# Optimization experiments

Measured on AMD Instinct MI355X. Metric: run time of the kernel, lower is better.

Reference implementation:

```python
import jax, jax.numpy as jnp
import numpy as np

B, N, D, S, H, ITERS = 128, 4096, 64, 7, 128, 3
EPS = 1e-8
LN_EPS = 1e-5


def _ln(x, g, b):
    mu = jnp.mean(x, axis=-1, keepdims=True)
    var = jnp.mean(jnp.square(x - mu), axis=-1, keepdims=True)
    return (x - mu) * jax.lax.rsqrt(var + LN_EPS) * g + b


def setup_inputs() -> dict:
    key = jax.random.key(0)
    ks = jax.random.split(key, 20)
    xav = lambda k, shp: jax.random.normal(k, shp, jnp.float32) * (2.0 / sum(shp[-2:])) ** 0.5
    inp = {
        "inputs": jax.random.normal(ks[0], (B, N, D), jnp.float32),
        "noise_bg": jax.random.normal(ks[1], (B, 1, D), jnp.float32),
        "noise_fg": jax.random.normal(ks[2], (B, S - 1, D), jnp.float32),
        "ln_in_g": jnp.ones((D,), jnp.float32), "ln_in_b": jnp.zeros((D,), jnp.float32),
        "ln_slot_g": jnp.ones((D,), jnp.float32), "ln_slot_b": jnp.zeros((D,), jnp.float32),
        "ln_mlp_g": jnp.ones((D,), jnp.float32), "ln_mlp_b": jnp.zeros((D,), jnp.float32),
        "Wq": xav(ks[3], (D, D)), "Wk": xav(ks[4], (D, D)), "Wv": xav(ks[5], (D, D)),
        "W_ih": xav(ks[6], (3 * D, D)), "W_hh": xav(ks[7], (3 * D, D)),
        "b_ih": jnp.zeros((3 * D,), jnp.float32), "b_hh": jnp.zeros((3 * D,), jnp.float32),
        "mlp_w1": xav(ks[8], (H, D)), "mlp_b1": jnp.zeros((H,), jnp.float32),
        "mlp_w2": xav(ks[9], (D, H)), "mlp_b2": jnp.zeros((D,), jnp.float32),
        "slots_bg_mu": xav(ks[10], (1, 1, D)),
        "slots_bg_log_sigma": xav(ks[11], (1, 1, D)),
        "slots_mu": xav(ks[12], (1, 1, D)),
        "slots_log_sigma": xav(ks[13], (1, 1, D)),
    }
    return inp


def _gru(x, h, W_ih, W_hh, b_ih, b_hh):
    # x, h: [M, D]; PyTorch GRUCell math, gate order r, z, n
    gi = x @ W_ih.T + b_ih
    gh = h @ W_hh.T + b_hh
    i_r, i_z, i_n = jnp.split(gi, 3, axis=-1)
    h_r, h_z, h_n = jnp.split(gh, 3, axis=-1)
    r = jax.nn.sigmoid(i_r + h_r)
    z = jax.nn.sigmoid(i_z + h_z)
    n = jnp.tanh(i_n + r * h_n)
    return (1.0 - z) * n + z * h


def reference(inputs, noise_bg, noise_fg, ln_in_g, ln_in_b, ln_slot_g, ln_slot_b,
              ln_mlp_g, ln_mlp_b, Wq, Wk, Wv, W_ih, W_hh, b_ih, b_hh,
              mlp_w1, mlp_b1, mlp_w2, mlp_b2,
              slots_bg_mu, slots_bg_log_sigma, slots_mu, slots_log_sigma):
    x = _ln(inputs, ln_in_g, ln_in_b)          # [B, N, D]
    k = jnp.einsum('bnd,ed->bne', x, Wk)       # [B, N, D]
    v = jnp.einsum('bnd,ed->bne', x, Wv)

    bg = slots_bg_mu + jnp.exp(slots_bg_log_sigma) * noise_bg   # [B, 1, D]
    fg = slots_mu + jnp.exp(slots_log_sigma) * noise_fg          # [B, S-1, D]
    slots = jnp.concatenate([bg, fg], axis=1)                    # [B, S, D]

    scale = D ** (-0.5)
    for _ in range(ITERS):
        slots_prev = slots
        s = _ln(slots, ln_slot_g, ln_slot_b)
        q = jnp.einsum('bsd,ed->bse', s, Wq)                     # [B, S, D]
        logits = scale * jnp.einsum('bnd,bsd->bns', k, q)        # [B, N, S]
        attn = jax.nn.softmax(logits, axis=-1) + EPS             # softmax over slots
        attn = attn / jnp.sum(attn, axis=1, keepdims=True)       # renorm over inputs
        updates = jnp.einsum('bns,bnd->bsd', attn, v)            # [B, S, D]
        h = _gru(updates.reshape(B * S, D), slots_prev.reshape(B * S, D),
                 W_ih, W_hh, b_ih, b_hh).reshape(B, S, D)
        m = _ln(h, ln_mlp_g, ln_mlp_b)
        m = jax.nn.relu(m @ mlp_w1.T + mlp_b1) @ mlp_w2.T + mlp_b2
        slots = h + m
    return slots
```

## Files before the change

kernel.cpp:

```cpp
#include <hip/hip_runtime.h>

#define BB 128
#define NN 4096
#define DD 64
#define SS 7
#define HH 128
#define N_ITERS 3
#define EPS_ATTN 1e-8f
#define LN_EPS 1e-5f

typedef unsigned short ushortT;
using short8  = __attribute__((ext_vector_type(8))) short;
using floatx4 = __attribute__((ext_vector_type(4))) float;

__device__ __forceinline__ float bf2f(unsigned u) {
    return __builtin_bit_cast(float, (u & 0xffffu) << 16);
}
__device__ __forceinline__ ushortT f2bf(float f) {
    unsigned x = __builtin_bit_cast(unsigned, f);
    x = x + 0x7fff + ((x >> 16) & 1);
    return (ushortT)(x >> 16);
}
__device__ __forceinline__ void wave_stats64(float x, float& mu, float& var) {
    float s1 = x, s2 = x * x;
#pragma unroll
    for (int off = 32; off > 0; off >>= 1) {
        s1 += __shfl_xor(s1, off);
        s2 += __shfl_xor(s2, off);
    }
    mu  = s1 * (1.f / 64.f);
    var = s2 * (1.f / 64.f) - mu * mu;
}

__global__ void prep_w(const float* __restrict__ Wih, const float* __restrict__ Whh,
                       const float* __restrict__ w1, const float* __restrict__ w2,
                       const float* __restrict__ Wv,
                       float* __restrict__ WihT, float* __restrict__ WhhT,
                       float* __restrict__ w1T, float* __restrict__ w2T,
                       float* __restrict__ WvT) {
    int i = blockIdx.x * 256 + threadIdx.x;
    if (i < 12288) {
        int e = i >> 6, d = i & 63;
        WihT[d * 192 + e] = Wih[i];
    } else if (i < 24576) {
        int j = i - 12288; int e = j >> 6, d = j & 63;
        WhhT[d * 192 + e] = Whh[j];
    } else if (i < 32768) {
        int j = i - 24576; int e = j >> 6, d = j & 63;
        w1T[d * 128 + e] = w1[j];
    } else if (i < 40960) {
        int j = i - 32768; int e = j >> 7, h = j & 127;
        w2T[h * 64 + e] = w2[j];
    } else if (i < 45056) {
        int j = i - 40960; int d = j >> 6, e = j & 63;
        WvT[e * 64 + d] = Wv[j];
    }
}

__global__ __launch_bounds__(256) void attn_kernel(
    int first,
    const float* __restrict__ x,
    const float* __restrict__ lng, const float* __restrict__ lnb,
    ushortT* __restrict__ xnf,
    const float* __restrict__ qkbuf,
    float* __restrict__ pxn_p, float* __restrict__ den_p) {
    int t = threadIdx.x;
    int ck = blockIdx.x, b = ck >> 5;
    int w = t >> 6, lane = t & 63, m = lane & 15, qd = lane >> 4;
    int sub = t & 3, rr = t >> 2;
    __shared__ float   qk_lds[7][68];
    __shared__ ushortT xnT[64][136];
    __shared__ ushortT p_lds[16][136];
    __shared__ float   den_w[4][8];

    unsigned xw[2][8];
    if (first) {
        float4 g4[4], b4[4];
#pragma unroll
        for (int c = 0; c < 4; ++c) {
            g4[c] = *reinterpret_cast<const float4*>(lng + sub * 16 + c * 4);
            b4[c] = *reinterpret_cast<const float4*>(lnb + sub * 16 + c * 4);
        }
#pragma unroll
        for (int pass = 0; pass < 2; ++pass) {
            const float* xr = x + ((long)ck * 128 + pass * 64 + rr) * 64 + sub * 16;
            float4 xa[4];
#pragma unroll
            for (int c = 0; c < 4; ++c)
                xa[c] = *reinterpret_cast<const float4*>(xr + c * 4);
            float s1 = 0.f, s2 = 0.f;
#pragma unroll
            for (int c = 0; c < 4; ++c) {
                s1 += xa[c].x + xa[c].y + xa[c].z + xa[c].w;
                s2 += xa[c].x * xa[c].x + xa[c].y * xa[c].y +
                      xa[c].z * xa[c].z + xa[c].w * xa[c].w;
            }
            s1 += __shfl_xor(s1, 1); s2 += __shfl_xor(s2, 1);
            s1 += __shfl_xor(s1, 2); s2 += __shfl_xor(s2, 2);
            float mu = s1 * (1.f / 64.f);
            float var = s2 * (1.f / 64.f) - mu * mu;
            float rs = rsqrtf(var + LN_EPS);
#pragma unroll
            for (int c = 0; c < 4; ++c) {
                float n0 = (xa[c].x - mu) * rs * g4[c].x + b4[c].x;
                float n1 = (xa[c].y - mu) * rs * g4[c].y + b4[c].y;
                float n2 = (xa[c].z - mu) * rs * g4[c].z + b4[c].z;
                float n3 = (xa[c].w - mu) * rs * g4[c].w + b4[c].w;
                xw[pass][c * 2]     = (unsigned)f2bf(n0) | ((unsigned)f2bf(n1) << 16);
                xw[pass][c * 2 + 1] = (unsigned)f2bf(n2) | ((unsigned)f2bf(n3) << 16);
            }
            ushortT* xp = xnf + (long)ck * 8192 + pass * 4096 + t * 16;
            *reinterpret_cast<uint4*>(xp) =
                make_uint4(xw[pass][0], xw[pass][1], xw[pass][2], xw[pass][3]);
            *reinterpret_cast<uint4*>(xp + 8) =
                make_uint4(xw[pass][4], xw[pass][5], xw[pass][6], xw[pass][7]);
        }
    } else {
#pragma unroll
        for (int pass = 0; pass < 2; ++pass) {
            const ushortT* xp = xnf + (long)ck * 8192 + pass * 4096 + t * 16;
            uint4 u0 = *reinterpret_cast<const uint4*>(xp);
            uint4 u1 = *reinterpret_cast<const uint4*>(xp + 8);
            xw[pass][0] = u0.x; xw[pass][1] = u0.y;
            xw[pass][2] = u0.z; xw[pass][3] = u0.w;
            xw[pass][4] = u1.x; xw[pass][5] = u1.y;
            xw[pass][6] = u1.z; xw[pass][7] = u1.w;
        }
    }
    for (int i = t; i < 448; i += 256) qk_lds[i >> 6][i & 63] = qkbuf[b * 448 + i];
    __syncthreads();

    float dreg0 = 0.f, dreg1 = 0.f;
    int s0 = sub * 2;
#pragma unroll
    for (int pass = 0; pass < 2; ++pass) {
        int row = pass * 64 + rr;
#pragma unroll
        for (int j = 0; j < 16; ++j)
            xnT[sub * 16 + j][row] =
                (ushortT)(xw[pass][j >> 1] >> ((j & 1) * 16));
        float kx[16];
#pragma unroll
        for (int j = 0; j < 8; ++j) {
            kx[2 * j]     = bf2f(xw[pass][j]);
            kx[2 * j + 1] = bf2f(xw[pass][j] >> 16);
        }
        float lg[7];
#pragma unroll
        for (int s = 0; s < 7; ++s) {
            const float4* qp = reinterpret_cast<const float4*>(&qk_lds[s][sub << 4]);
            float acc = 0.f;
#pragma unroll
            for (int c = 0; c < 4; ++c) {
                float4 qv = qp[c];
                acc += kx[c * 4 + 0] * qv.x + kx[c * 4 + 1] * qv.y +
                       kx[c * 4 + 2] * qv.z + kx[c * 4 + 3] * qv.w;
            }
            lg[s] = acc;
        }
#pragma unroll
        for (int s = 0; s < 7; ++s) {
            lg[s] += __shfl_xor(lg[s], 1);
            lg[s] += __shfl_xor(lg[s], 2);
        }
        float mx = lg[0];
#pragma unroll
        for (int s = 1; s < 7; ++s) mx = fmaxf(mx, lg[s]);
        float sum = 0.f, ps[7];
#pragma unroll
        for (int s = 0; s < 7; ++s) { ps[s] = __expf(lg[s] - mx); sum += ps[s]; }
        float inv = 1.f / sum;
        float p0 = 0.f, p1 = 0.f;
#pragma unroll
        for (int s = 0; s < 7; ++s) {
            float pv = ps[s] * inv + EPS_ATTN;
            if (s == s0)     p0 = pv;
            if (s == s0 + 1) p1 = pv;
        }
        ushortT pb0 = f2bf(p0);
        p_lds[s0][row] = pb0;
        dreg0 += bf2f(pb0);
        if (sub < 3) {
            ushortT pb1 = f2bf(p1);
            p_lds[s0 + 1][row] = pb1;
            dreg1 += bf2f(pb1);
        }
    }
#pragma unroll
    for (int off = 4; off < 64; off <<= 1) {
        dreg0 += __shfl_xor(dreg0, off);
        dreg1 += __shfl_xor(dreg1, off);
    }
    if (lane < 4) {
        den_w[w][2 * lane] = dreg0;
        if (lane < 3) den_w[w][2 * lane + 1] = dreg1;
    }
    __syncthreads();

    floatx4 acc = (floatx4){0.f, 0.f, 0.f, 0.f};
#pragma unroll
    for (int ks = 0; ks < 4; ++ks) {
        short8 af = *reinterpret_cast<const short8*>(&p_lds[m][ks * 32 + qd * 8]);
        short8 bf = *reinterpret_cast<const short8*>(&xnT[w * 16 + m][ks * 32 + qd * 8]);
        acc = __builtin_amdgcn_mfma_f32_16x16x32_bf16(af, bf, acc, 0, 0, 0);
    }
#pragma unroll
    for (int r = 0; r < 4; ++r) {
        int s = qd * 4 + r;
        if (s < 7) pxn_p[((long)ck * 7 + s) * 64 + w * 16 + m] = acc[r];
    }
    if (t < 7) den_p[ck * 8 + t] = den_w[0][t] + den_w[1][t] + den_w[2][t] + den_w[3][t];
}

__global__ __launch_bounds__(448) void slot_update_q(
    int mode,
    const float* __restrict__ pxn_p, const float* __restrict__ den_p,
    float* __restrict__ slots,
    const float* __restrict__ nbg, const float* __restrict__ nfg,
    const float* __restrict__ bgmu, const float* __restrict__ bgls,
    const float* __restrict__ fmu, const float* __restrict__ fls,
    const float* __restrict__ WihT, const float* __restrict__ WhhT,
    const float* __restrict__ bih, const float* __restrict__ bhh,
    const float* __restrict__ lng, const float* __restrict__ lnb,
    const float* __restrict__ w1T, const float* __restrict__ b1,
    const float* __restrict__ w2T, const float* __restrict__ b2,
    const float* __restrict__ WvT, const float* __restrict__ Wk,
    const float* __restrict__ Wq,
    const float* __restrict__ sg, const float* __restrict__ sb,
    float* __restrict__ qkbuf, float* __restrict__ outp) {
    int b = blockIdx.x, t = threadIdx.x, s = t >> 6, l = t & 63;
    __shared__ float WqT[64 * 65];
    __shared__ float pxnL[7][64], updL[7][64], hprevL[7][64], mnL[7][64],
                     xnL[7][64], qL[7][64], m1L[7][128];
    if (mode != 2)
        for (int i = t; i < 4096; i += 448)
            WqT[(i & 63) * 65 + (i >> 6)] = Wq[i];
    float res;
    if (mode == 0) {
        float v;
        if (s == 0) v = bgmu[l] + __expf(bgls[l]) * nbg[b * 64 + l];
        else        v = fmu[l]  + __expf(fls[l])  * nfg[(b * 6 + s - 1) * 64 + l];
        res = v;
        __syncthreads();
    } else {
        float psum = 0.f, dsum = 0.f;
#pragma unroll 4
        for (int c = 0; c < 32; ++c) {
            psum += pxn_p[((long)(b * 32 + c) * 7 + s) * 64 + l];
            dsum += den_p[(b * 32 + c) * 8 + s];
        }
        pxnL[s][l] = psum;
        float hp = slots[(b * 7 + s) * 64 + l];
        hprevL[s][l] = hp;
        float nm = 0.f;
#pragma unroll 8
        for (int e = 0; e < 64; ++e) nm += pxnL[s][e] * WvT[e * 64 + l];
        updL[s][l] = nm / dsum;
        __syncthreads();
        float gi0 = bih[l], gi1 = bih[64 + l], gi2 = bih[128 + l];
        float gh0 = bhh[l], gh1 = bhh[64 + l], gh2 = bhh[128 + l];
#pragma unroll 8
        for (int d = 0; d < 64; ++d) {
            float u = updL[s][d], hh = hprevL[s][d];
            gi0 += u * WihT[d * 192 + l];
            gi1 += u * WihT[d * 192 + 64 + l];
            gi2 += u * WihT[d * 192 + 128 + l];
            gh0 += hh * WhhT[d * 192 + l];
            gh1 += hh * WhhT[d * 192 + 64 + l];
            gh2 += hh * WhhT[d * 192 + 128 + l];
        }
        float r = 1.f / (1.f + __expf(-(gi0 + gh0)));
        float z = 1.f / (1.f + __expf(-(gi1 + gh1)));
        float n = tanhf(gi2 + r * gh2);
        float h = (1.f - z) * n + z * hp;
        float mu, var;
        wave_stats64(h, mu, var);
        mnL[s][l] = (h - mu) * rsqrtf(var + LN_EPS) * lng[l] + lnb[l];
        float a0 = b1[l], a1 = b1[64 + l];
#pragma unroll 8
        for (int d = 0; d < 64; ++d) {
            float mv = mnL[s][d];
            a0 += mv * w1T[d * 128 + l];
            a1 += mv * w1T[d * 128 + 64 + l];
        }
        m1L[s][l]      = fmaxf(a0, 0.f);
        m1L[s][64 + l] = fmaxf(a1, 0.f);
        float a2 = b2[l];
#pragma unroll 8
        for (int h2 = 0; h2 < 128; ++h2) a2 += m1L[s][h2] * w2T[h2 * 64 + l];
        res = h + a2;
    }
    slots[(b * 7 + s) * 64 + l] = res;
    if (mode == 2) {
        outp[(b * 7 + s) * 64 + l] = res;
        return;
    }
    float mu, var;
    wave_stats64(res, mu, var);
    xnL[s][l] = (res - mu) * rsqrtf(var + LN_EPS) * sg[l] + sb[l];
    float qv = 0.f;
#pragma unroll 8
    for (int d = 0; d < 64; ++d) qv += xnL[s][d] * WqT[d * 65 + l];
    qL[s][l] = qv * 0.125f;
    float qk = 0.f;
#pragma unroll 8
    for (int e = 0; e < 64; ++e) qk += qL[s][e] * Wk[e * 64 + l];
    qkbuf[(b * 7 + s) * 64 + l] = qk;
}

extern "C" void kernel_launch(void* const* d_in, const int* in_sizes, int n_in,
                              void* d_out, int out_size, void* d_ws, size_t ws_size,
                              hipStream_t stream) {
    const float* inputs    = (const float*)d_in[0];
    const float* noise_bg  = (const float*)d_in[1];
    const float* noise_fg  = (const float*)d_in[2];
    const float* ln_in_g   = (const float*)d_in[3];
    const float* ln_in_b   = (const float*)d_in[4];
    const float* ln_slot_g = (const float*)d_in[5];
    const float* ln_slot_b = (const float*)d_in[6];
    const float* ln_mlp_g  = (const float*)d_in[7];
    const float* ln_mlp_b  = (const float*)d_in[8];
    const float* Wq        = (const float*)d_in[9];
    const float* Wk        = (const float*)d_in[10];
    const float* Wv        = (const float*)d_in[11];
    const float* W_ih      = (const float*)d_in[12];
    const float* W_hh      = (const float*)d_in[13];
    const float* b_ih      = (const float*)d_in[14];
    const float* b_hh      = (const float*)d_in[15];
    const float* mlp_w1    = (const float*)d_in[16];
    const float* mlp_b1    = (const float*)d_in[17];
    const float* mlp_w2    = (const float*)d_in[18];
    const float* mlp_b2    = (const float*)d_in[19];
    const float* sbg_mu    = (const float*)d_in[20];
    const float* sbg_ls    = (const float*)d_in[21];
    const float* s_mu      = (const float*)d_in[22];
    const float* s_ls      = (const float*)d_in[23];

    char* ws = (char*)d_ws;
    size_t off = 0;
    auto alloc = [&](size_t bytes) {
        void* p = ws + off;
        off += (bytes + 255) & ~(size_t)255;
        return p;
    };
    ushortT* xnf   = (ushortT*)alloc((size_t)BB * NN * 64 * 2);
    float* slots   = (float*)alloc(57344 * 4);
    float* qkbuf   = (float*)alloc(57344 * 4);
    float* pxn_p   = (float*)alloc((size_t)4096 * 7 * 64 * 4);
    float* den_p   = (float*)alloc(4096 * 8 * 4);
    float* WihT    = (float*)alloc(12288 * 4);
    float* WhhT    = (float*)alloc(12288 * 4);
    float* w1T     = (float*)alloc(8192 * 4);
    float* w2T     = (float*)alloc(8192 * 4);
    float* WvT     = (float*)alloc(4096 * 4);
    if (off > ws_size) return;

    prep_w<<<176, 256, 0, stream>>>(W_ih, W_hh, mlp_w1, mlp_w2, Wv,
                                    WihT, WhhT, w1T, w2T, WvT);
    slot_update_q<<<128, 448, 0, stream>>>(0, pxn_p, den_p, slots,
                                           noise_bg, noise_fg, sbg_mu, sbg_ls,
                                           s_mu, s_ls, WihT, WhhT, b_ih, b_hh,
                                           ln_mlp_g, ln_mlp_b, w1T, mlp_b1,
                                           w2T, mlp_b2, WvT, Wk, Wq,
                                           ln_slot_g, ln_slot_b,
                                           qkbuf, (float*)d_out);
    for (int it = 0; it < N_ITERS; ++it) {
        attn_kernel<<<4096, 256, 0, stream>>>((it == 0) ? 1 : 0,
                                              inputs, ln_in_g, ln_in_b,
                                              xnf, qkbuf, pxn_p, den_p);
        slot_update_q<<<128, 448, 0, stream>>>((it == N_ITERS - 1) ? 2 : 1,
                                               pxn_p, den_p, slots,
                                               noise_bg, noise_fg, sbg_mu, sbg_ls,
                                               s_mu, s_ls, WihT, WhhT, b_ih, b_hh,
                                               ln_mlp_g, ln_mlp_b, w1T, mlp_b1,
                                               w2T, mlp_b2, WvT, Wk, Wq,
                                               ln_slot_g, ln_slot_b,
                                               qkbuf, (float*)d_out);
    }
}
```

Before: 382.6 us.

## Compute attention logits with MFMA and split slot update into per-slot blocks

The attention kernel now computes key-query logits with bf16 MFMA instructions in place of scalar dot products plus shuffles. To support this, the row-to-lane layout is changed to an MFMA-friendly tile layout, and the transposed LDS buffer gets a 140 stride. The slot update kernel moves from 128 blocks of 448 threads to 896 blocks of 192 threads, one per slot, with WqT precomputed in prep_w. The qk buffer is stored transposed and padded to 8 slots. The logits now use a bf16-rounded query, which can shift precision slightly.

```diff
diff --git a/kernel.cpp b/kernel.cpp
--- a/kernel.cpp
+++ b/kernel.cpp
@@ -12,6 +12,7 @@
 typedef unsigned short ushortT;
 using short8  = __attribute__((ext_vector_type(8))) short;
 using floatx4 = __attribute__((ext_vector_type(4))) float;
+using uint4v  = __attribute__((ext_vector_type(4))) unsigned;
 
 __device__ __forceinline__ float bf2f(unsigned u) {
     return __builtin_bit_cast(float, (u & 0xffffu) << 16);
@@ -34,10 +35,10 @@
 
 __global__ void prep_w(const float* __restrict__ Wih, const float* __restrict__ Whh,
                        const float* __restrict__ w1, const float* __restrict__ w2,
-                       const float* __restrict__ Wv,
+                       const float* __restrict__ Wv, const float* __restrict__ Wq,
                        float* __restrict__ WihT, float* __restrict__ WhhT,
                        float* __restrict__ w1T, float* __restrict__ w2T,
-                       float* __restrict__ WvT) {
+                       float* __restrict__ WvT, float* __restrict__ WqT) {
     int i = blockIdx.x * 256 + threadIdx.x;
     if (i < 12288) {
         int e = i >> 6, d = i & 63;
@@ -54,6 +55,9 @@
     } else if (i < 45056) {
         int j = i - 40960; int d = j >> 6, e = j & 63;
         WvT[e * 64 + d] = Wv[j];
+    } else if (i < 49152) {
+        int j = i - 45056; int d = j >> 6, e = j & 63;
+        WqT[j] = Wq[e * 64 + d];
     }
 }
 
@@ -62,157 +66,181 @@
     const float* __restrict__ x,
     const float* __restrict__ lng, const float* __restrict__ lnb,
     ushortT* __restrict__ xnf,
-    const float* __restrict__ qkbuf,
+    const float* __restrict__ qkT,
     float* __restrict__ pxn_p, float* __restrict__ den_p) {
     int t = threadIdx.x;
     int ck = blockIdx.x, b = ck >> 5;
     int w = t >> 6, lane = t & 63, m = lane & 15, qd = lane >> 4;
-    int sub = t & 3, rr = t >> 2;
-    __shared__ float   qk_lds[7][68];
-    __shared__ ushortT xnT[64][136];
+    __shared__ float   qk_lds[512];
+    __shared__ ushortT xnT[64 * 140];
     __shared__ ushortT p_lds[16][136];
     __shared__ float   den_w[4][8];
 
+    for (int i = t; i < 512; i += 256) qk_lds[i] = qkT[b * 512 + i];
+
     unsigned xw[2][8];
     if (first) {
-        float4 g4[4], b4[4];
-#pragma unroll
-        for (int c = 0; c < 4; ++c) {
-            g4[c] = *reinterpret_cast<const float4*>(lng + sub * 16 + c * 4);
-            b4[c] = *reinterpret_cast<const float4*>(lnb + sub * 16 + c * 4);
-        }
-#pragma unroll
-        for (int pass = 0; pass < 2; ++pass) {
-            const float* xr = x + ((long)ck * 128 + pass * 64 + rr) * 64 + sub * 16;
-            float4 xa[4];
-#pragma unroll
-            for (int c = 0; c < 4; ++c)
-                xa[c] = *reinterpret_cast<const float4*>(xr + c * 4);
+        float4 g4[2][2], b4[2][2];
+#pragma unroll
+        for (int c = 0; c < 2; ++c) {
+            g4[c][0] = *reinterpret_cast<const float4*>(lng + c * 32 + qd * 8);
+            g4[c][1] = *reinterpret_cast<const float4*>(lng + c * 32 + qd * 8 + 4);
+            b4[c][0] = *reinterpret_cast<const float4*>(lnb + c * 32 + qd * 8);
+            b4[c][1] = *reinterpret_cast<const float4*>(lnb + c * 32 + qd * 8 + 4);
+        }
+#pragma unroll
+        for (int tile = 0; tile < 2; ++tile) {
+            long R = (long)ck * 128 + w * 32 + tile * 16 + m;
+            float4 xa[2][2];
+#pragma unroll
+            for (int c = 0; c < 2; ++c) {
+                xa[c][0] = *reinterpret_cast<const float4*>(x + R * 64 + c * 32 + qd * 8);
+                xa[c][1] = *reinterpret_cast<const float4*>(x + R * 64 + c * 32 + qd * 8 + 4);
+            }
             float s1 = 0.f, s2 = 0.f;
 #pragma unroll
-            for (int c = 0; c < 4; ++c) {
-                s1 += xa[c].x + xa[c].y + xa[c].z + xa[c].w;
-                s2 += xa[c].x * xa[c].x + xa[c].y * xa[c].y +
-                      xa[c].z * xa[c].z + xa[c].w * xa[c].w;
-            }
-            s1 += __shfl_xor(s1, 1); s2 += __shfl_xor(s2, 1);
-            s1 += __shfl_xor(s1, 2); s2 += __shfl_xor(s2, 2);
+            for (int c = 0; c < 2; ++c)
+#pragma unroll
+                for (int h = 0; h < 2; ++h) {
+                    float4 v = xa[c][h];
+                    s1 += v.x + v.y + v.z + v.w;
+                    s2 += v.x * v.x + v.y * v.y + v.z * v.z + v.w * v.w;
+                }
+            s1 += __shfl_xor(s1, 16); s2 += __shfl_xor(s2, 16);
+            s1 += __shfl_xor(s1, 32); s2 += __shfl_xor(s2, 32);
             float mu = s1 * (1.f / 64.f);
             float var = s2 * (1.f / 64.f) - mu * mu;
             float rs = rsqrtf(var + LN_EPS);
 #pragma unroll
-            for (int c = 0; c < 4; ++c) {
-                float n0 = (xa[c].x - mu) * rs * g4[c].x + b4[c].x;
-                float n1 = (xa[c].y - mu) * rs * g4[c].y + b4[c].y;
-                float n2 = (xa[c].z - mu) * rs * g4[c].z + b4[c].z;
-                float n3 = (xa[c].w - mu) * rs * g4[c].w + b4[c].w;
-                xw[pass][c * 2]     = (unsigned)f2bf(n0) | ((unsigned)f2bf(n1) << 16);
-                xw[pass][c * 2 + 1] = (unsigned)f2bf(n2) | ((unsigned)f2bf(n3) << 16);
-            }
-            ushortT* xp = xnf + (long)ck * 8192 + pass * 4096 + t * 16;
+            for (int c = 0; c < 2; ++c)
+#pragma unroll
+                for (int h = 0; h < 2; ++h) {
+                    float n0 = (xa[c][h].x - mu) * rs * g4[c][h].x + b4[c][h].x;
+                    float n1 = (xa[c][h].y - mu) * rs * g4[c][h].y + b4[c][h].y;
+                    float n2 = (xa[c][h].z - mu) * rs * g4[c][h].z + b4[c][h].z;
+                    float n3 = (xa[c][h].w - mu) * rs * g4[c][h].w + b4[c][h].w;
+                    xw[tile][c * 4 + h * 2]     = (unsigned)f2bf(n0) | ((unsigned)f2bf(n1) << 16);
+                    xw[tile][c * 4 + h * 2 + 1] = (unsigned)f2bf(n2) | ((unsigned)f2bf(n3) << 16);
+                }
+            ushortT* xp = xnf + (long)ck * 8192 + w * 2048 + tile * 1024 + lane * 16;
             *reinterpret_cast<uint4*>(xp) =
-                make_uint4(xw[pass][0], xw[pass][1], xw[pass][2], xw[pass][3]);
+                make_uint4(xw[tile][0], xw[tile][1], xw[tile][2], xw[tile][3]);
             *reinterpret_cast<uint4*>(xp + 8) =
-                make_uint4(xw[pass][4], xw[pass][5], xw[pass][6], xw[pass][7]);
+                make_uint4(xw[tile][4], xw[tile][5], xw[tile][6], xw[tile][7]);
         }
     } else {
 #pragma unroll
-        for (int pass = 0; pass < 2; ++pass) {
-            const ushortT* xp = xnf + (long)ck * 8192 + pass * 4096 + t * 16;
+        for (int tile = 0; tile < 2; ++tile) {
+            const ushortT* xp = xnf + (long)ck * 8192 + w * 2048 + tile * 1024 + lane * 16;
             uint4 u0 = *reinterpret_cast<const uint4*>(xp);
             uint4 u1 = *reinterpret_cast<const uint4*>(xp + 8);
-            xw[pass][0] = u0.x; xw[pass][1] = u0.y;
-            xw[pass][2] = u0.z; xw[pass][3] = u0.w;
-            xw[pass][4] = u1.x; xw[pass][5] = u1.y;
-            xw[pass][6] = u1.z; xw[pass][7] = u1.w;
-        }
-    }
-    for (int i = t; i < 448; i += 256) qk_lds[i >> 6][i & 63] = qkbuf[b * 448 + i];
+            xw[tile][0] = u0.x; xw[tile][1] = u0.y; xw[tile][2] = u0.z; xw[tile][3] = u0.w;
+            xw[tile][4] = u1.x; xw[tile][5] = u1.y; xw[tile][6] = u1.z; xw[tile][7] = u1.w;
+        }
+    }
     __syncthreads();
 
-    float dreg0 = 0.f, dreg1 = 0.f;
-    int s0 = sub * 2;
-#pragma unroll
-    for (int pass = 0; pass < 2; ++pass) {
-        int row = pass * 64 + rr;
-#pragma unroll
-        for (int j = 0; j < 16; ++j)
-            xnT[sub * 16 + j][row] =
-                (ushortT)(xw[pass][j >> 1] >> ((j & 1) * 16));
-        float kx[16];
-#pragma unroll
-        for (int j = 0; j < 8; ++j) {
-            kx[2 * j]     = bf2f(xw[pass][j]);
-            kx[2 * j + 1] = bf2f(xw[pass][j] >> 16);
-        }
-        float lg[7];
-#pragma unroll
-        for (int s = 0; s < 7; ++s) {
-            const float4* qp = reinterpret_cast<const float4*>(&qk_lds[s][sub << 4]);
-            float acc = 0.f;
-#pragma unroll
-            for (int c = 0; c < 4; ++c) {
-                float4 qv = qp[c];
-                acc += kx[c * 4 + 0] * qv.x + kx[c * 4 + 1] * qv.y +
-                       kx[c * 4 + 2] * qv.z + kx[c * 4 + 3] * qv.w;
-            }
-            lg[s] = acc;
-        }
-#pragma unroll
-        for (int s = 0; s < 7; ++s) {
-            lg[s] += __shfl_xor(lg[s], 1);
-            lg[s] += __shfl_xor(lg[s], 2);
-        }
-        float mx = lg[0];
-#pragma unroll
-        for (int s = 1; s < 7; ++s) mx = fmaxf(mx, lg[s]);
-        float sum = 0.f, ps[7];
-#pragma unroll
-        for (int s = 0; s < 7; ++s) { ps[s] = __expf(lg[s] - mx); sum += ps[s]; }
+    short8 aq[2];
+#pragma unroll
+    for (int c = 0; c < 2; ++c) {
+        short8 a = {};
+        if (m < 8) {
+#pragma unroll
+            for (int j = 0; j < 8; ++j)
+                a[j] = (short)f2bf(qk_lds[(c * 32 + qd * 8 + j) * 8 + m]);
+        }
+        aq[c] = a;
+    }
+
+    float dreg03[4] = {0.f, 0.f, 0.f, 0.f};
+    float dreg46[3] = {0.f, 0.f, 0.f};
+#pragma unroll
+    for (int tile = 0; tile < 2; ++tile) {
+        int row = w * 32 + tile * 16 + m;
+#pragma unroll
+        for (int c = 0; c < 2; ++c)
+#pragma unroll
+            for (int j = 0; j < 8; ++j) {
+                int e = c * 32 + qd * 8 + j;
+                xnT[e * 140 + row] =
+                    (ushortT)(xw[tile][c * 4 + (j >> 1)] >> ((j & 1) * 16));
+            }
+        uint4v b0 = {xw[tile][0], xw[tile][1], xw[tile][2], xw[tile][3]};
+        uint4v b1 = {xw[tile][4], xw[tile][5], xw[tile][6], xw[tile][7]};
+        floatx4 acc = (floatx4){0.f, 0.f, 0.f, 0.f};
+        acc = __builtin_amdgcn_mfma_f32_16x16x32_bf16(aq[0],
+                  __builtin_bit_cast(short8, b0), acc, 0, 0, 0);
+        acc = __builtin_amdgcn_mfma_f32_16x16x32_bf16(aq[1],
+                  __builtin_bit_cast(short8, b1), acc, 0, 0, 0);
+        float own[4], par[4];
+#pragma unroll
+        for (int r = 0; r < 4; ++r) { own[r] = acc[r]; par[r] = __shfl_xor(acc[r], 16); }
+        float lgA[4], lgB[4];
+#pragma unroll
+        for (int r = 0; r < 4; ++r) {
+            lgA[r] = (qd & 1) ? par[r] : own[r];
+            lgB[r] = (qd & 1) ? own[r] : par[r];
+        }
+        float mx = fmaxf(fmaxf(fmaxf(lgA[0], lgA[1]), fmaxf(lgA[2], lgA[3])),
+                         fmaxf(fmaxf(lgB[0], lgB[1]), lgB[2]));
+        float eA[4], eB[3], sum = 0.f;
+#pragma unroll
+        for (int r = 0; r < 4; ++r) { eA[r] = __expf(lgA[r] - mx); sum += eA[r]; }
+#pragma unroll
+        for (int r = 0; r < 3; ++r) { eB[r] = __expf(lgB[r] - mx); sum += eB[r]; }
         float inv = 1.f / sum;
-        float p0 = 0.f, p1 = 0.f;
-#pragma unroll
-        for (int s = 0; s < 7; ++s) {
-            float pv = ps[s] * inv + EPS_ATTN;
-            if (s == s0)     p0 = pv;
-            if (s == s0 + 1) p1 = pv;
-        }
-        ushortT pb0 = f2bf(p0);
-        p_lds[s0][row] = pb0;
-        dreg0 += bf2f(pb0);
-        if (sub < 3) {
-            ushortT pb1 = f2bf(p1);
-            p_lds[s0 + 1][row] = pb1;
-            dreg1 += bf2f(pb1);
-        }
-    }
-#pragma unroll
-    for (int off = 4; off < 64; off <<= 1) {
-        dreg0 += __shfl_xor(dreg0, off);
-        dreg1 += __shfl_xor(dreg1, off);
-    }
-    if (lane < 4) {
-        den_w[w][2 * lane] = dreg0;
-        if (lane < 3) den_w[w][2 * lane + 1] = dreg1;
+        if (qd == 0) {
+#pragma unroll
+            for (int r = 0; r < 4; ++r) {
+                ushortT pb = f2bf(eA[r] * inv + EPS_ATTN);
+                p_lds[r][row] = pb;
+                dreg03[r] += bf2f(pb);
+            }
+        } else if (qd == 1) {
+#pragma unroll
+            for (int r = 0; r < 3; ++r) {
+                ushortT pb = f2bf(eB[r] * inv + EPS_ATTN);
+                p_lds[4 + r][row] = pb;
+                dreg46[r] += bf2f(pb);
+            }
+        }
+    }
+#pragma unroll
+    for (int off = 1; off < 16; off <<= 1) {
+#pragma unroll
+        for (int r = 0; r < 4; ++r) dreg03[r] += __shfl_xor(dreg03[r], off);
+#pragma unroll
+        for (int r = 0; r < 3; ++r) dreg46[r] += __shfl_xor(dreg46[r], off);
+    }
+    if (m == 0 && qd == 0) {
+#pragma unroll
+        for (int r = 0; r < 4; ++r) den_w[w][r] = dreg03[r];
+    } else if (m == 0 && qd == 1) {
+#pragma unroll
+        for (int r = 0; r < 3; ++r) den_w[w][4 + r] = dreg46[r];
     }
     __syncthreads();
 
-    floatx4 acc = (floatx4){0.f, 0.f, 0.f, 0.f};
+    floatx4 acc2 = (floatx4){0.f, 0.f, 0.f, 0.f};
 #pragma unroll
     for (int ks = 0; ks < 4; ++ks) {
-        short8 af = *reinterpret_cast<const short8*>(&p_lds[m][ks * 32 + qd * 8]);
-        short8 bf = *reinterpret_cast<const short8*>(&xnT[w * 16 + m][ks * 32 + qd * 8]);
-        acc = __builtin_amdgcn_mfma_f32_16x16x32_bf16(af, bf, acc, 0, 0, 0);
+        short8 ap = *reinterpret_cast<const short8*>(&p_lds[m][ks * 32 + qd * 8]);
+        const ushortT* xp = xnT + (w * 16 + m) * 140 + ks * 32 + qd * 8;
+        uint2 u0 = *reinterpret_cast<const uint2*>(xp);
+        uint2 u1 = *reinterpret_cast<const uint2*>(xp + 4);
+        uint4v bb = {u0.x, u0.y, u1.x, u1.y};
+        acc2 = __builtin_amdgcn_mfma_f32_16x16x32_bf16(ap,
+                   __builtin_bit_cast(short8, bb), acc2, 0, 0, 0);
     }
 #pragma unroll
     for (int r = 0; r < 4; ++r) {
         int s = qd * 4 + r;
-        if (s < 7) pxn_p[((long)ck * 7 + s) * 64 + w * 16 + m] = acc[r];
+        if (s < 7) pxn_p[((long)ck * 7 + s) * 64 + w * 16 + m] = acc2[r];
     }
     if (t < 7) den_p[ck * 8 + t] = den_w[0][t] + den_w[1][t] + den_w[2][t] + den_w[3][t];
 }
 
-__global__ __launch_bounds__(448) void slot_update_q(
+__global__ __launch_bounds__(192) void slot_update_q(
     int mode,
     const float* __restrict__ pxn_p, const float* __restrict__ den_p,
     float* __restrict__ slots,
@@ -224,88 +252,99 @@
     const float* __restrict__ lng, const float* __restrict__ lnb,
     const float* __restrict__ w1T, const float* __restrict__ b1,
     const float* __restrict__ w2T, const float* __restrict__ b2,
-    const float* __restrict__ WvT, const float* __restrict__ Wk,
-    const float* __restrict__ Wq,
+    const float* __restrict__ WvT, const float* __restrict__ WqT,
+    const float* __restrict__ Wk,
     const float* __restrict__ sg, const float* __restrict__ sb,
-    float* __restrict__ qkbuf, float* __restrict__ outp) {
-    int b = blockIdx.x, t = threadIdx.x, s = t >> 6, l = t & 63;
-    __shared__ float WqT[64 * 65];
-    __shared__ float pxnL[7][64], updL[7][64], hprevL[7][64], mnL[7][64],
-                     xnL[7][64], qL[7][64], m1L[7][128];
-    if (mode != 2)
-        for (int i = t; i < 4096; i += 448)
-            WqT[(i & 63) * 65 + (i >> 6)] = Wq[i];
-    float res;
+    float* __restrict__ qkT, float* __restrict__ outp) {
+    int bs = blockIdx.x, t = threadIdx.x;
+    int b = bs / 7, s = bs % 7;
+    __shared__ float pxnL[64], hprevL[64], updL[64], giL[192], ghL[192],
+                     mnL[64], m1L[128], xnL[64], qL[64];
+    float res = 0.f, dsum = 0.f;
     if (mode == 0) {
-        float v;
-        if (s == 0) v = bgmu[l] + __expf(bgls[l]) * nbg[b * 64 + l];
-        else        v = fmu[l]  + __expf(fls[l])  * nfg[(b * 6 + s - 1) * 64 + l];
-        res = v;
+        if (t < 64) {
+            if (s == 0) res = bgmu[t] + __expf(bgls[t]) * nbg[b * 64 + t];
+            else        res = fmu[t]  + __expf(fls[t])  * nfg[(b * 6 + s - 1) * 64 + t];
+        }
+    } else {
+        if (t < 64) {
+            float psum = 0.f;
+#pragma unroll 8
+            for (int c = 0; c < 32; ++c) {
+                psum += pxn_p[((long)(b * 32 + c) * 7 + s) * 64 + t];
+                dsum += den_p[(b * 32 + c) * 8 + s];
+            }
+            pxnL[t]   = psum;
+            hprevL[t] = slots[bs * 64 + t];
+        }
         __syncthreads();
-    } else {
-        float psum = 0.f, dsum = 0.f;
-#pragma unroll 4
-        for (int c = 0; c < 32; ++c) {
-            psum += pxn_p[((long)(b * 32 + c) * 7 + s) * 64 + l];
-            dsum += den_p[(b * 32 + c) * 8 + s];
-        }
-        pxnL[s][l] = psum;
-        float hp = slots[(b * 7 + s) * 64 + l];
-        hprevL[s][l] = hp;
-        float nm = 0.f;
-#pragma unroll 8
-        for (int e = 0; e < 64; ++e) nm += pxnL[s][e] * WvT[e * 64 + l];
-        updL[s][l] = nm / dsum;
+        if (t < 64) {
+            float nm = 0.f;
+#pragma unroll 8
+            for (int e = 0; e < 64; ++e) nm += pxnL[e] * WvT[e * 64 + t];
+            updL[t] = nm / dsum;
+        }
         __syncthreads();
-        float gi0 = bih[l], gi1 = bih[64 + l], gi2 = bih[128 + l];
-        float gh0 = bhh[l], gh1 = bhh[64 + l], gh2 = bhh[128 + l];
-#pragma unroll 8
-        for (int d = 0; d < 64; ++d) {
-            float u = updL[s][d], hh = hprevL[s][d];
-            gi0 += u * WihT[d * 192 + l];
-            gi1 += u * WihT[d * 192 + 64 + l];
-            gi2 += u * WihT[d * 192 + 128 + l];
-            gh0 += hh * WhhT[d * 192 + l];
-            gh1 += hh * WhhT[d * 192 + 64 + l];
-            gh2 += hh * WhhT[d * 192 + 128 + l];
-        }
-        float r = 1.f / (1.f + __expf(-(gi0 + gh0)));
-        float z = 1.f / (1.f + __expf(-(gi1 + gh1)));
-        float n = tanhf(gi2 + r * gh2);
-        float h = (1.f - z) * n + z * hp;
+        {
+            float a = bih[t], h2 = bhh[t];
+#pragma unroll 8
+            for (int d = 0; d < 64; ++d) {
+                a  += updL[d]   * WihT[d * 192 + t];
+                h2 += hprevL[d] * WhhT[d * 192 + t];
+            }
+            giL[t] = a; ghL[t] = h2;
+        }
+        __syncthreads();
+        if (t < 64) {
+            float r = 1.f / (1.f + __expf(-(giL[t] + ghL[t])));
+            float z = 1.f / (1.f + __expf(-(giL[64 + t] + ghL[64 + t])));
+            float n = tanhf(giL[128 + t] + r * ghL[128 + t]);
+            float h = (1.f - z) * n + z * hprevL[t];
+            res = h;
+            float mu, var;
+            wave_stats64(h, mu, var);
+            mnL[t] = (h - mu) * rsqrtf(var + LN_EPS) * lng[t] + lnb[t];
+        }
+        __syncthreads();
+        if (t < 128) {
+            float a = b1[t];
+#pragma unroll 8
+            for (int d = 0; d < 64; ++d) a += mnL[d] * w1T[d * 128 + t];
+            m1L[t] = fmaxf(a, 0.f);
+        }
+        __syncthreads();
+        if (t < 64) {
+            float a = b2[t];
+#pragma unroll 8
+            for (int h2 = 0; h2 < 128; ++h2) a += m1L[h2] * w2T[h2 * 64 + t];
+            res += a;
+        }
+    }
+    if (t < 64) slots[bs * 64 + t] = res;
+    if (mode == 2) {
+        if (t < 64) outp[bs * 64 + t] = res;
+        return;
+    }
+    if (t < 64) {
         float mu, var;
-        wave_stats64(h, mu, var);
-        mnL[s][l] = (h - mu) * rsqrtf(var + LN_EPS) * lng[l] + lnb[l];
-        float a0 = b1[l], a1 = b1[64 + l];
-#pragma unroll 8
-        for (int d = 0; d < 64; ++d) {
-            float mv = mnL[s][d];
-            a0 += mv * w1T[d * 128 + l];
-            a1 += mv * w1T[d * 128 + 64 + l];
-        }
-        m1L[s][l]      = fmaxf(a0, 0.f);
-        m1L[s][64 + l] = fmaxf(a1, 0.f);
-        float a2 = b2[l];
-#pragma unroll 8
-        for (int h2 = 0; h2 < 128; ++h2) a2 += m1L[s][h2] * w2T[h2 * 64 + l];
-        res = h + a2;
-    }
-    slots[(b * 7 + s) * 64 + l] = res;
-    if (mode == 2) {
-        outp[(b * 7 + s) * 64 + l] = res;
-        return;
-    }
-    float mu, var;
-    wave_stats64(res, mu, var);
-    xnL[s][l] = (res - mu) * rsqrtf(var + LN_EPS) * sg[l] + sb[l];
-    float qv = 0.f;
-#pragma unroll 8
-    for (int d = 0; d < 64; ++d) qv += xnL[s][d] * WqT[d * 65 + l];
-    qL[s][l] = qv * 0.125f;
-    float qk = 0.f;
-#pragma unroll 8
-    for (int e = 0; e < 64; ++e) qk += qL[s][e] * Wk[e * 64 + l];
-    qkbuf[(b * 7 + s) * 64 + l] = qk;
+        wave_stats64(res, mu, var);
+        xnL[t] = (res - mu) * rsqrtf(var + LN_EPS) * sg[t] + sb[t];
+    }
+    __syncthreads();
+    if (t < 64) {
+        float q = 0.f;
+#pragma unroll 8
+        for (int d = 0; d < 64; ++d) q += xnL[d] * WqT[d * 64 + t];
+        qL[t] = q * 0.125f;
+    }
+    __syncthreads();
+    if (t < 64) {
+        float qk = 0.f;
+#pragma unroll 8
+        for (int e = 0; e < 64; ++e) qk += qL[e] * Wk[e * 64 + t];
+        qkT[b * 512 + t * 8 + s] = qk;
+        if (s == 0) qkT[b * 512 + t * 8 + 7] = 0.f;
+    }
 }
 
 extern "C" void kernel_launch(void* const* d_in, const int* in_sizes, int n_in,
@@ -345,7 +384,7 @@
     };
     ushortT* xnf   = (ushortT*)alloc((size_t)BB * NN * 64 * 2);
     float* slots   = (float*)alloc(57344 * 4);
-    float* qkbuf   = (float*)alloc(57344 * 4);
+    float* qkT     = (float*)alloc((size_t)BB * 512 * 4);
     float* pxn_p   = (float*)alloc((size_t)4096 * 7 * 64 * 4);
     float* den_p   = (float*)alloc(4096 * 8 * 4);
     float* WihT    = (float*)alloc(12288 * 4);
@@ -353,28 +392,29 @@
     float* w1T     = (float*)alloc(8192 * 4);
     float* w2T     = (float*)alloc(8192 * 4);
     float* WvT     = (float*)alloc(4096 * 4);
+    float* WqT     = (float*)alloc(4096 * 4);
     if (off > ws_size) return;
 
-    prep_w<<<176, 256, 0, stream>>>(W_ih, W_hh, mlp_w1, mlp_w2, Wv,
-                                    WihT, WhhT, w1T, w2T, WvT);
-    slot_update_q<<<128, 448, 0, stream>>>(0, pxn_p, den_p, slots,
+    prep_w<<<192, 256, 0, stream>>>(W_ih, W_hh, mlp_w1, mlp_w2, Wv, Wq,
+                                    WihT, WhhT, w1T, w2T, WvT, WqT);
+    slot_update_q<<<896, 192, 0, stream>>>(0, pxn_p, den_p, slots,
                                            noise_bg, noise_fg, sbg_mu, sbg_ls,
                                            s_mu, s_ls, WihT, WhhT, b_ih, b_hh,
                                            ln_mlp_g, ln_mlp_b, w1T, mlp_b1,
-                                           w2T, mlp_b2, WvT, Wk, Wq,
+                                           w2T, mlp_b2, WvT, WqT, Wk,
                                            ln_slot_g, ln_slot_b,
-                                           qkbuf, (float*)d_out);
+                                           qkT, (float*)d_out);
     for (int it = 0; it < N_ITERS; ++it) {
         attn_kernel<<<4096, 256, 0, stream>>>((it == 0) ? 1 : 0,
                                               inputs, ln_in_g, ln_in_b,
-                                              xnf, qkbuf, pxn_p, den_p);
-        slot_update_q<<<128, 448, 0, stream>>>((it == N_ITERS - 1) ? 2 : 1,
+                                              xnf, qkT, pxn_p, den_p);
+        slot_update_q<<<896, 192, 0, stream>>>((it == N_ITERS - 1) ? 2 : 1,
                                                pxn_p, den_p, slots,
                                                noise_bg, noise_fg, sbg_mu, sbg_ls,
                                                s_mu, s_ls, WihT, WhhT, b_ih, b_hh,
                                                ln_mlp_g, ln_mlp_b, w1T, mlp_b1,
-                                               w2T, mlp_b2, WvT, Wk, Wq,
+                                               w2T, mlp_b2, WvT, WqT, Wk,
                                                ln_slot_g, ln_slot_b,
-                                               qkbuf, (float*)d_out);
-    }
-}
+                                               qkT, (float*)d_out);
+    }
+}
```

After: 359.8 us. 6.0% less time.
